# Performance work log

Hardware: AMD Instinct MI355X
Metric: run time of the kernel (lower is better)

The kernel has to match this reference:

```python
import jax, jax.numpy as jnp
import numpy as np

BS, L, ED = 4, 2048, 1024
D = ED // 2          # time_embedding_dim = 512
ANG_HID = D // 4     # AngleEmb hidden = 128
T_MAX = 1010


def _gelu(x):
    return jax.nn.gelu(x, approximate=False)  # torch F.gelu default = exact erf


def _time_embed(t, w1, b1, w2, b2):
    # sinusoidal (diffusion-style, base 10000) + 2-layer MLP; t: [N] float
    half = D // 2
    freqs = jnp.exp(-jnp.log(10000.0) * jnp.arange(half, dtype=jnp.float32) / half)
    a = t[:, None] * freqs[None, :]
    e = jnp.concatenate([jnp.sin(a), jnp.cos(a)], axis=-1)  # [N, D]
    return _gelu(e @ w1 + b1) @ w2 + b2


def _cal_dist(p, aa_seq):
    # p: [bs, L, 3]; ragged per-segment mean pairwise distance.
    # Segments run (cls_idx+1 .. eos_idx-1]; token 0 = cls, token 2 = eos.
    cls = (aa_seq == 0)
    eos = (aa_seq == 2)
    seg = jnp.cumsum(cls.astype(jnp.int32), axis=1)                       # segment id
    valid = (seg > jnp.cumsum(eos.astype(jnp.int32), axis=1)) & ~cls & ~eos
    same = (seg[:, :, None] == seg[:, None, :]) & valid[:, :, None] & valid[:, None, :]
    diff = p[:, :, None, :] - p[:, None, :, :]                            # [bs,L,L,3]
    sq = jnp.sum(diff * diff, axis=-1)
    d = jnp.where(sq > 0, jnp.sqrt(jnp.where(sq > 0, sq, 1.0)), 0.0)      # safe norm
    cnt = jnp.sum(same, axis=-1)                                           # segment size (incl self)
    dist = jnp.where(valid, jnp.sum(d * same, axis=-1) / jnp.maximum(cnt, 1), 0.0)
    return dist[..., None]                                                 # [bs,L,1]


def setup_inputs() -> dict:
    key = jax.random.key(0)
    ks = jax.random.split(key, 26)
    # build ragged aa_seq: repeated [cls=0, residues in [3,25), eos=2], pad token 1
    rng = np.random.default_rng(0)
    aa = np.ones((BS, L), dtype=np.int64)
    pad = np.ones((BS, L), dtype=bool)
    for b in range(BS):
        i = 0
        while i < L - 8:
            seg = int(rng.integers(16, 64))
            seg = min(seg, L - i - 2)
            aa[b, i] = 0
            aa[b, i + 1:i + 1 + seg] = rng.integers(3, 25, size=seg)
            aa[b, i + 1 + seg] = 2
            pad[b, i:i + 2 + seg] = False
            i += seg + 2
    s = 0.05
    inp = {
        "pos": jax.random.normal(ks[0], (BS, L, 3, 3), jnp.float32) * 5.0,
        "angle": jax.random.uniform(ks[1], (BS, L, 6), jnp.float32, -3.14, 3.14),
        "padding_mask": jnp.asarray(pad),
        "mask_aa": jax.random.bernoulli(ks[2], 0.15, (BS, L, 1)),
        "mask_pos": jax.random.bernoulli(ks[3], 0.15, (BS, L, 1)),
        "mask_angle": jax.random.bernoulli(ks[4], 0.15, (BS, L, 1)),
        "angle_mask": jax.random.bernoulli(ks[5], 0.9, (BS, L, 3)),
        "bond_angle_mask": jax.random.bernoulli(ks[6], 0.9, (BS, L, 3)),
        "time_pos": jax.random.randint(ks[7], (BS, L), 0, T_MAX).astype(jnp.float32),
        "time_angle": jnp.zeros((BS, L, 6), jnp.float32),  # overwritten in fwd (dim-2 path)
        "aa_seq": jnp.asarray(aa),
        # parameters ([in, out] layout; torch Linear bias=False unless noted)
        "ang_w1": jax.random.normal(ks[8], (1, ANG_HID), jnp.float32) * 0.5,
        "ang_w2": jax.random.normal(ks[9], (ANG_HID, D), jnp.float32) * s,
        "pos_w1": jax.random.normal(ks[10], (1, 1), jnp.float32) * 0.5,
        "pos_w2": jax.random.normal(ks[11], (1, D), jnp.float32) * s,
        "te_w1": jax.random.normal(ks[12], (D, D), jnp.float32) * s,
        "te_b1": jnp.zeros((D,), jnp.float32),
        "te_w2": jax.random.normal(ks[13], (D, D), jnp.float32) * s,
        "te_b2": jnp.zeros((D,), jnp.float32),
        "angproj_w": jax.random.normal(ks[14], (6 * D, D), jnp.float32) * s,
        "angproj_b": jnp.zeros((D,), jnp.float32),
        "posproj_w": jax.random.normal(ks[15], (D, D), jnp.float32) * s,
        "posproj_b": jnp.zeros((D,), jnp.float32),
        "cls_w": jax.random.normal(ks[16], (1, ED), jnp.float32) * s,
        "eos_w": jax.random.normal(ks[17], (1, ED), jnp.float32) * s,
        "unkang_w": jax.random.normal(ks[18], (1, D), jnp.float32) * s,
        "unkpos_w": jax.random.normal(ks[19], (1, D), jnp.float32) * s,
    }
    return inp


def reference(pos, angle, padding_mask, mask_aa, mask_pos, mask_angle,
              angle_mask, bond_angle_mask, time_pos, time_angle, aa_seq,
              ang_w1, ang_w2, pos_w1, pos_w2,
              te_w1, te_b1, te_w2, te_b2,
              angproj_w, angproj_b, posproj_w, posproj_b,
              cls_w, eos_w, unkang_w, unkpos_w):
    bs, nnode, _ = angle.shape
    amask = jnp.concatenate([angle_mask[:, :, :3], bond_angle_mask], axis=-1)  # [bs,L,6]
    ang = jnp.where(amask, angle, 0.0).reshape(bs, -1, 1)                      # [bs,6L,1]
    cls_mask = (aa_seq == 0)[..., None]
    eos_mask = (aa_seq == 2)[..., None]

    angle_feat = _gelu(ang @ ang_w1) @ ang_w2                                  # [bs,6L,D]
    angle_feat = jnp.where(amask.reshape(bs, -1, 1), angle_feat, unkang_w[0])

    dist = _cal_dist(pos[:, :, 1, :], aa_seq)                                  # [bs,L,1]
    pos_feat = _gelu(dist @ pos_w1) @ pos_w2                                   # [bs,L,D]
    pos_mask = ~(cls_mask | eos_mask)
    pos_feat = jnp.where(pos_mask, pos_feat, unkpos_w[0])

    # time_pos is 2-D -> [bs,L,1]; time_angle := time_pos repeated to [bs,L,6]
    ta = jnp.where(amask, jnp.broadcast_to(time_pos[..., None], (bs, nnode, 6)), 0.0)
    temb_pos = _time_embed(time_pos.reshape(-1), te_w1, te_b1, te_w2, te_b2).reshape(bs, -1, D)
    temb_ang = _time_embed(ta.reshape(-1), te_w1, te_b1, te_w2, te_b2).reshape(bs, -1, D)
    t0_emb = _time_embed(jnp.zeros((1,), jnp.float32), te_w1, te_b1, te_w2, te_b2)[0]  # all-zero t rows are identical

    t_mask = mask_angle & ~cls_mask & ~eos_mask                                # [bs,L,1]
    temb_ang = jnp.where(jnp.tile(t_mask, (1, 6, 1)), temb_ang, t0_emb)        # torch .repeat(1,6,1)
    temb_pos = jnp.where(t_mask, temb_pos, t0_emb)
    angle_feat = angle_feat + temb_ang
    pos_feat = pos_feat + temb_pos

    angle_feat = angle_feat.reshape(bs, nnode, 6 * D) @ angproj_w + angproj_b  # [bs,L,D]
    pos_feat = pos_feat @ posproj_w + posproj_b                                # [bs,L,D]
    node = jnp.concatenate([angle_feat, pos_feat], axis=-1)                    # [bs,L,ED]
    node = jnp.where(cls_mask, cls_w[0], node)
    node = jnp.where(eos_mask, eos_w[0], node)
    node = jnp.where(padding_mask[..., None], 0.0, node)
    return node
```

## Files before the change

### kernel.cpp

```cpp
#include <hip/hip_runtime.h>
#include <hip/hip_bf16.h>
#include <cstdint>
#include <cstddef>

#define BSZ 4
#define SEQL 2048
#define DDIM 512
#define AHID 128
#define NROWS (BSZ*SEQL)
#define NANG (NROWS*6)
#define KCAT 768
#define NTT 1024

typedef __attribute__((ext_vector_type(8))) short short8;
typedef __attribute__((ext_vector_type(4))) float f32x4;
typedef __hip_bfloat16 bf16;

__device__ __forceinline__ float gelu_f(float x){
  return 0.5f * x * (1.0f + erff(x * 0.7071067811865475f));
}

__device__ __forceinline__ void gload16(const void* g, void* l){
  __builtin_amdgcn_global_load_lds(
      (const __attribute__((address_space(1))) unsigned int*)g,
      (__attribute__((address_space(3))) unsigned int*)l,
      16, 0, 0);
}

__device__ __forceinline__ unsigned int packbf2(float a, float b){
  __hip_bfloat16 ha = __float2bfloat16(a), hb = __float2bfloat16(b);
  return (unsigned int)(*(unsigned short*)&ha) | ((unsigned int)(*(unsigned short*)&hb) << 16);
}

__global__ void pre_kernel(const int* __restrict__ aa, const float* __restrict__ pos,
                           float4* __restrict__ pk,
                           const float* __restrict__ te_b2,
                           const float* __restrict__ angproj_w, const float* __restrict__ posproj_w,
                           const float* __restrict__ unkang, const float* __restrict__ pos_w2,
                           float* __restrict__ U, float* __restrict__ Wg,
                           float* __restrict__ qb){
  int blk = blockIdx.x, tid = threadIdx.x;
  if (blk == 0){
    int b = tid >> 6, lane = tid & 63;
    const int CH = SEQL/64;
    int base = b*SEQL + lane*CH;
    int av[CH];
    int lc=0, le=0;
    #pragma unroll
    for (int i=0;i<CH;i++){ int a=aa[base+i]; av[i]=a; lc += (a==0); le += (a==2); }
    int pc=lc, pe=le;
    #pragma unroll
    for (int off=1; off<64; off<<=1){
      int tc = __shfl_up(pc, off);
      int te = __shfl_up(pe, off);
      if (lane >= off){ pc += tc; pe += te; }
    }
    int c = pc - lc, eo = pe - le;
    #pragma unroll
    for (int i=0;i<CH;i++){
      int a = av[i];
      c += (a==0); eo += (a==2);
      bool valid = (c>eo) && (a!=0) && (a!=2);
      float4 q;
      q.x = pos[(size_t)(base+i)*9+3];
      q.y = pos[(size_t)(base+i)*9+4];
      q.z = pos[(size_t)(base+i)*9+5];
      q.w = valid ? (float)c : -1.f;
      pk[base+i] = q;
    }
    return;
  }
  int q = blk - 1;
  if (q < 96){
    int j = q >> 4, rem = q & 15;
    int nc = rem >> 3, dc = rem & 7;
    int n = nc*256 + tid, d0 = dc*64;
    float s = 0.f;
    #pragma unroll 4
    for (int i=0;i<64;i++)
      s += unkang[d0+i] * angproj_w[((size_t)(j*512 + d0+i))*512 + n];
    atomicAdd(U + j*512 + n, s);
    return;
  }
  q -= 96;
  if (q < 16){
    int nc = q >> 3, dc = q & 7;
    int n = nc*256 + tid, d0 = dc*64;
    float s = 0.f;
    #pragma unroll 4
    for (int i=0;i<64;i++)
      s += pos_w2[d0+i] * posproj_w[(size_t)(d0+i)*512 + n];
    atomicAdd(Wg + n, s);
    return;
  }
  q -= 16;
  {
    int j = q >> 4, rem = q & 15;
    int nc = rem >> 3, dc = rem & 7;
    int n = nc*256 + tid, d0 = dc*64;
    const float* W = (j<6) ? (angproj_w + (size_t)(j*512)*512) : posproj_w;
    float s = 0.f;
    #pragma unroll 4
    for (int i=0;i<64;i++)
      s += te_b2[d0+i] * W[(size_t)(d0+i)*512 + n];
    atomicAdd(qb + j*512 + n, s);
  }
}

#define NB_ANGH 3072
#define NB_SIN  256
#define NB_TR   2208
#define NB_PREP 32
#define NB_DIST 2048
#define NB_TOTAL (NB_ANGH+NB_SIN+NB_TR+NB_PREP+NB_DIST)

__device__ void do_transpose(const float* __restrict__ W, bf16* __restrict__ Wt,
                             int K, int q, float (*tsh)[33]){
  int k0 = (q >> 4)*32, n0 = (q & 15)*32;
  int tx = threadIdx.x & 31, ty = threadIdx.x >> 5;
  #pragma unroll
  for (int i=0;i<32;i+=8)
    tsh[ty+i][tx] = W[(size_t)(k0+ty+i)*512 + n0+tx];
  __syncthreads();
  #pragma unroll
  for (int i=0;i<32;i+=8)
    Wt[(size_t)(n0+ty+i)*K + k0+tx] = __float2bfloat16(tsh[tx][ty+i]);
}

__global__ void prologue_kernel(const float* __restrict__ angle,
                                const int* __restrict__ angm, const int* __restrict__ bondm,
                                const int* __restrict__ mask_angle, const int* __restrict__ aa,
                                const int* __restrict__ padm,
                                const float* __restrict__ ang_w1,
                                const float* __restrict__ te_w1, const float* __restrict__ te_w2,
                                const float* __restrict__ ang_w2, const float* __restrict__ angproj_w,
                                const float* __restrict__ posproj_w,
                                const float4* __restrict__ pk,
                                bf16* __restrict__ Hang, bf16* __restrict__ et,
                                bf16* __restrict__ tw1t, bf16* __restrict__ apjt,
                                bf16* __restrict__ ppjt, bf16* __restrict__ w2b,
                                bf16* __restrict__ tw2b,
                                unsigned char* __restrict__ amb, unsigned char* __restrict__ scb,
                                float* __restrict__ dist){
  __shared__ float tsh[32][33];
  int blk = blockIdx.x;
  int tid = threadIdx.x;
  if (blk < NB_ANGH){
    int gidx = blk*256 + tid;
    int row = gidx >> 4;
    int kb = (gidx & 15) * 8;
    int bq = row / (SEQL*6);
    int rr = row - bq*(SEQL*6);
    int l = rr / 6, j = rr - l*6;
    int bl = bq*SEQL + l;
    int m = (j<3) ? angm[bl*3+j] : bondm[bl*3+(j-3)];
    float x = m ? angle[bl*6+j] : 0.f;
    float4 w0 = *(const float4*)(ang_w1+kb);
    float4 w1v = *(const float4*)(ang_w1+kb+4);
    uint4 st;
    st.x = packbf2(gelu_f(x*w0.x),  gelu_f(x*w0.y));
    st.y = packbf2(gelu_f(x*w0.z),  gelu_f(x*w0.w));
    st.z = packbf2(gelu_f(x*w1v.x), gelu_f(x*w1v.y));
    st.w = packbf2(gelu_f(x*w1v.z), gelu_f(x*w1v.w));
    *(uint4*)(Hang + (size_t)row*AHID + kb) = st;
    return;
  }
  blk -= NB_ANGH;
  if (blk < NB_SIN){
    int gidx = blk*256 + tid;
    int row = gidx >> 6;
    int db = (gidx & 63) * 8;
    float t = (float)row;
    float v[8];
    #pragma unroll
    for (int i=0;i<8;i++){
      int d = db + i;
      int k = d & 255;
      float f = exp2f(-0.05190512648262f * (float)k);
      float a = t * f;
      v[i] = (d < 256) ? __sinf(a) : __cosf(a);
    }
    uint4 st;
    st.x = packbf2(v[0],v[1]); st.y = packbf2(v[2],v[3]);
    st.z = packbf2(v[4],v[5]); st.w = packbf2(v[6],v[7]);
    *(uint4*)(et + (size_t)row*DDIM + db) = st;
    return;
  }
  blk -= NB_SIN;
  if (blk < NB_TR){
    if (blk < 256)       do_transpose(te_w1, tw1t, 512, blk, tsh);
    else if (blk < 1792) do_transpose(angproj_w, apjt, 3072, blk-256, tsh);
    else if (blk < 2048) do_transpose(posproj_w, ppjt, 512, blk-1792, tsh);
    else if (blk < 2080){
      int gidx = (blk-2048)*256 + tid;
      float4 a0 = *(const float4*)(ang_w2 + (size_t)gidx*8);
      float4 a1 = *(const float4*)(ang_w2 + (size_t)gidx*8 + 4);
      uint4 st;
      st.x = packbf2(a0.x,a0.y); st.y = packbf2(a0.z,a0.w);
      st.z = packbf2(a1.x,a1.y); st.w = packbf2(a1.z,a1.w);
      *(uint4*)(w2b + (size_t)gidx*8) = st;
    } else {
      int gidx = (blk-2080)*256 + tid;
      float4 a0 = *(const float4*)(te_w2 + (size_t)gidx*8);
      float4 a1 = *(const float4*)(te_w2 + (size_t)gidx*8 + 4);
      uint4 st;
      st.x = packbf2(a0.x,a0.y); st.y = packbf2(a0.z,a0.w);
      st.z = packbf2(a1.x,a1.y); st.w = packbf2(a1.z,a1.w);
      *(uint4*)(tw2b + (size_t)gidx*8) = st;
    }
    return;
  }
  blk -= NB_TR;
  if (blk < NB_PREP){
    int bl = blk*256 + tid;
    int b = bl >> 11, l = bl & (SEQL-1);
    int a = aa[bl];
    bool rowOK = (a!=0) && (a!=2) && (padm[bl]==0);
    int ab=0, sb=0;
    #pragma unroll
    for (int j=0;j<6;j++){
      int am = (j<3) ? angm[bl*3+j] : bondm[bl*3+(j-3)];
      int rr = l*6 + j;
      int bl2 = b*SEQL + (rr & (SEQL-1));
      int a2 = aa[bl2];
      bool tm = mask_angle[bl2] && (a2!=0) && (a2!=2);
      bool qs = tm && (am!=0) && rowOK;
      if (am)  ab |= (1<<j);
      if (qs)  sb |= (1<<j);
    }
    if ((mask_angle[bl]!=0) && rowOK) sb |= 64;
    amb[bl] = (unsigned char)ab;
    scb[bl] = (unsigned char)sb;
    return;
  }
  blk -= NB_PREP;
  {
    int gw = blk*4 + (tid >> 6);
    int lane = tid & 63;
    float4 c = pk[gw];
    float out = 0.f;
    if (c.w >= 0.f){
      int rowbase = (gw >> 11) << 11;
      int jlo = gw - 64; if (jlo < rowbase) jlo = rowbase;
      int jhi = gw + 64; if (jhi >= rowbase + SEQL) jhi = rowbase + SEQL - 1;
      float s = 0.f, cnt = 0.f;
      for (int j = gw - 64 + lane; j <= jhi; j += 64){
        if (j < jlo) continue;
        float4 q = pk[j];
        if (q.w == c.w){
          float dx = c.x-q.x, dy = c.y-q.y, dz = c.z-q.z;
          float sq = dx*dx+dy*dy+dz*dz;
          s += (sq>0.f) ? sqrtf(sq) : 0.f;
          cnt += 1.f;
        }
      }
      #pragma unroll
      for (int off=32; off>0; off>>=1){
        s   += __shfl_down(s, off);
        cnt += __shfl_down(cnt, off);
      }
      out = s / fmaxf(cnt, 1.f);
    }
    if (lane==0) dist[gw] = out;
  }
}

struct EpiArgs {
  const float* bias;
  const unsigned char* amb;
  const unsigned char* scb;
  const float* U;
  const float* Y;
  const float* tp;
  const int* aa;
  const int* pad;
  const float* cls;
  const float* eos;
  float* outF;
  bf16* outB;
  int cnt;
  int coloff;
  int ldc;
};

#define STG_BYTES 12288
#define SMEM_BYTES 49152

template<int EPI>
__device__ __forceinline__ void gemm_core(const char* gA, const char* gB,
                                          int K, int bm, int bn, const EpiArgs& ea, char* smem){
  const int tid = threadIdx.x;
  const int w = tid >> 6, lane = tid & 63;
  const bool doB = (w < 4);
  const int wm = (w>>1)*32, wn = (w&1)*32;
  const int lm = lane & 15, kq = lane >> 4;
  const int sw = kq ^ ((lm>>1)&3);
  const int NT = K >> 5;

  f32x4 acc[2][2];
  #pragma unroll
  for (int i=0;i<2;i++)
    #pragma unroll
    for (int j=0;j<2;j++) acc[i][j] = (f32x4){0.f,0.f,0.f,0.f};

  #pragma unroll
  for (int s=0; s<3; ++s){
    char* base = smem + s*STG_BYTES;
    gload16(gA + (size_t)s*64, base + w*1024);
    if (doB) gload16(gB + (size_t)s*64, base + 8192 + w*1024);
  }

  for (int t = 0; t < NT; ++t){
    char* cur = smem + (t&3)*STG_BYTES;
    if (t+3 < NT){
      char* nxt = smem + ((t+3)&3)*STG_BYTES;
      gload16(gA + (size_t)(t+3)*64, nxt + w*1024);
      if (doB) gload16(gB + (size_t)(t+3)*64, nxt + 8192 + w*1024);
    }
    int ia = NT-1-t; if (ia > 3) ia = 3;
    if (doB){
      if      (ia==3) __asm__ volatile("s_waitcnt vmcnt(6)" ::: "memory");
      else if (ia==2) __asm__ volatile("s_waitcnt vmcnt(4)" ::: "memory");
      else if (ia==1) __asm__ volatile("s_waitcnt vmcnt(2)" ::: "memory");
      else            __asm__ volatile("s_waitcnt vmcnt(0)" ::: "memory");
    } else {
      if      (ia==3) __asm__ volatile("s_waitcnt vmcnt(3)" ::: "memory");
      else if (ia==2) __asm__ volatile("s_waitcnt vmcnt(2)" ::: "memory");
      else if (ia==1) __asm__ volatile("s_waitcnt vmcnt(1)" ::: "memory");
      else            __asm__ volatile("s_waitcnt vmcnt(0)" ::: "memory");
    }
    __builtin_amdgcn_s_barrier();
    short8 af[2], bfr[2];
    #pragma unroll
    for (int tt=0;tt<2;tt++) af[tt]  = *(const short8*)(cur + (wm+tt*16+lm)*64 + sw*16);
    #pragma unroll
    for (int tt=0;tt<2;tt++) bfr[tt] = *(const short8*)(cur + 8192 + (wn+tt*16+lm)*64 + sw*16);
    #pragma unroll
    for (int mt=0;mt<2;mt++)
      #pragma unroll
      for (int nt=0;nt<2;nt++)
        acc[mt][nt] = __builtin_amdgcn_mfma_f32_16x16x32_bf16(af[mt], bfr[nt], acc[mt][nt], 0, 0, 0);
    __builtin_amdgcn_s_barrier();
  }

  float* eps = (float*)smem + w*576;
  const int erow = lane >> 2;
  const int ecg  = (lane & 3) * 8;
  #pragma unroll
  for (int mt=0; mt<2; mt++){
    #pragma unroll
    for (int nt=0; nt<2; nt++)
      #pragma unroll
      for (int rr=0; rr<4; rr++)
        eps[(kq*4+rr)*36 + nt*16 + lm] = acc[mt][nt][rr];
    __asm__ volatile("s_waitcnt lgkmcnt(0)" ::: "memory");
    float4 t0v = *(float4*)(eps + erow*36 + ecg);
    float4 t1v = *(float4*)(eps + erow*36 + ecg + 4);
    float v[8] = {t0v.x,t0v.y,t0v.z,t0v.w,t1v.x,t1v.y,t1v.z,t1v.w};
    __asm__ volatile("s_waitcnt lgkmcnt(0)" ::: "memory");
    int row = bm + wm + mt*16 + erow;
    int col = bn + wn + ecg;

    if (EPI==0 || EPI==1){
      float4 b0 = *(const float4*)(ea.bias+col), b1 = *(const float4*)(ea.bias+col+4);
      float bb[8] = {b0.x,b0.y,b0.z,b0.w,b1.x,b1.y,b1.z,b1.w};
      #pragma unroll
      for (int i=0;i<8;i++){
        v[i] += bb[i];
        if (EPI==0) v[i] = gelu_f(v[i]);
      }
      uint4 st;
      st.x = packbf2(v[0],v[1]); st.y = packbf2(v[2],v[3]);
      st.z = packbf2(v[4],v[5]); st.w = packbf2(v[6],v[7]);
      *(uint4*)(ea.outB + (size_t)row*ea.ldc + col) = st;
    } else if (EPI==4){
      uint4 st;
      st.x = packbf2(v[0],v[1]); st.y = packbf2(v[2],v[3]);
      st.z = packbf2(v[4],v[5]); st.w = packbf2(v[6],v[7]);
      *(uint4*)(ea.outB + (size_t)row*ea.ldc + col + ea.coloff) = st;
    } else if (EPI==5){
      float4 b0 = *(const float4*)(ea.bias+col), b1 = *(const float4*)(ea.bias+col+4);
      v[0]+=b0.x; v[1]+=b0.y; v[2]+=b0.z; v[3]+=b0.w;
      v[4]+=b1.x; v[5]+=b1.y; v[6]+=b1.z; v[7]+=b1.w;
      int ab = ea.amb[row], sc = ea.scb[row];
      int trow = (int)ea.tp[row];
      #pragma unroll
      for (int j=0;j<6;j++){
        float mU = ((ab>>j)&1) ? 0.f : 1.f;
        const float* Up = ea.U + j*512 + col;
        float4 u0=*(const float4*)Up, u1=*(const float4*)(Up+4);
        int idx = ((sc>>j)&1) ? trow : 0;
        const float* yp = ea.Y + ((size_t)j*NTT + idx)*512 + col;
        float4 y0=*(const float4*)yp, y1=*(const float4*)(yp+4);
        v[0]+=mU*u0.x+y0.x; v[1]+=mU*u0.y+y0.y;
        v[2]+=mU*u0.z+y0.z; v[3]+=mU*u0.w+y0.w;
        v[4]+=mU*u1.x+y1.x; v[5]+=mU*u1.y+y1.y;
        v[6]+=mU*u1.z+y1.z; v[7]+=mU*u1.w+y1.w;
      }
      int a = ea.aa[row];
      if (a==0){
        float4 c0 = *(const float4*)(ea.cls+col), c1 = *(const float4*)(ea.cls+col+4);
        v[0]=c0.x;v[1]=c0.y;v[2]=c0.z;v[3]=c0.w;v[4]=c1.x;v[5]=c1.y;v[6]=c1.z;v[7]=c1.w;
      } else if (a==2){
        float4 c0 = *(const float4*)(ea.eos+col), c1 = *(const float4*)(ea.eos+col+4);
        v[0]=c0.x;v[1]=c0.y;v[2]=c0.z;v[3]=c0.w;v[4]=c1.x;v[5]=c1.y;v[6]=c1.z;v[7]=c1.w;
      }
      if (ea.pad[row]){
        #pragma unroll
        for (int i=0;i<8;i++) v[i]=0.f;
      }
      *(float4*)(ea.outF + (size_t)row*ea.ldc + col)     = make_float4(v[0],v[1],v[2],v[3]);
      *(float4*)(ea.outF + (size_t)row*ea.ldc + col + 4) = make_float4(v[4],v[5],v[6],v[7]);
    } else {
      if (row < ea.cnt){
        float4 b0 = *(const float4*)(ea.bias+col), b1 = *(const float4*)(ea.bias+col+4);
        v[0]+=b0.x; v[1]+=b0.y; v[2]+=b0.z; v[3]+=b0.w;
        v[4]+=b1.x; v[5]+=b1.y; v[6]+=b1.z; v[7]+=b1.w;
        float* dst = ea.outF + (size_t)row*ea.ldc + col;
        *(float4*)dst     = make_float4(v[0],v[1],v[2],v[3]);
        *(float4*)(dst+4) = make_float4(v[4],v[5],v[6],v[7]);
      }
    }
  }
}

__device__ __forceinline__ void mk_addrs(const bf16* A, size_t lda, int bm,
                                         const bf16* Bt, size_t ldb, int bn,
                                         const char*& gA, const char*& gB){
  int tid = threadIdx.x;
  int w = tid >> 6, lane = tid & 63;
  int r = w*16 + (lane>>2);
  int cg = (lane&3) ^ ((r>>1)&3);
  gA = (const char*)(A + (size_t)(bm+r)*lda + cg*8);
  gB = (const char*)(Bt + (size_t)(bn+r)*ldb + cg*8);
}

__launch_bounds__(512, 8)
__global__ void te1_wcat_q_kernel(const bf16* __restrict__ et, const bf16* __restrict__ tw1t,
                                  EpiArgs eaH,
                                  const bf16* __restrict__ apjt, const bf16* __restrict__ ppjt,
                                  const bf16* __restrict__ w2b, const bf16* __restrict__ tw2b,
                                  EpiArgs eaW, bf16* __restrict__ QT){
  __shared__ __align__(16) char smem[SMEM_BYTES];
  int id = blockIdx.x;
  const char *gA, *gB;
  if (id < 64){
    int m = id >> 3, n = id & 7;
    mk_addrs(et, 512, m*128, tw1t, 512, n*64, gA, gB);
    gemm_core<0>(gA, gB, 512, m*128, n*64, eaH, smem);
  } else if (id < 112){
    int q = id - 64;
    int j = q >> 3, m = (q >> 1) & 3, n = q & 1;
    mk_addrs(apjt, 3072, m*128, w2b, 512, n*64, gA, gB);
    gA += (size_t)j*512*2;
    eaW.coloff = j*128;
    gemm_core<4>(gA, gB, 512, m*128, n*64, eaW, smem);
  } else {
    int q = id - 112;
    int j = q >> 5, rem = q & 31;
    int m = rem >> 3, n = rem & 7;
    if (j < 6){
      mk_addrs(apjt, 3072, m*128, tw2b, 512, n*64, gA, gB);
      gA += (size_t)j*512*2;
    } else {
      mk_addrs(ppjt, 512, m*128, tw2b, 512, n*64, gA, gB);
    }
    EpiArgs ea{};
    ea.outB = QT + (size_t)j*DDIM*DDIM; ea.ldc = DDIM; ea.coloff = 0;
    gemm_core<4>(gA, gB, 512, m*128, n*64, ea, smem);
  }
}

__launch_bounds__(512, 8)
__global__ void yt_kernel(const bf16* __restrict__ H1, const bf16* __restrict__ QT,
                          const float* __restrict__ qb, float* __restrict__ YT){
  __shared__ __align__(16) char smem[SMEM_BYTES];
  int id = blockIdx.x;
  int jj = id >> 6, rem = id & 63;
  int mt = rem >> 3, nt = rem & 7;
  const char *gA, *gB;
  mk_addrs(H1, 512, mt*128, QT + (size_t)jj*DDIM*DDIM, 512, nt*64, gA, gB);
  EpiArgs ea{};
  ea.bias = qb + jj*512;
  ea.cnt = NTT;
  ea.outF = YT + (size_t)jj*NTT*512;
  ea.ldc = 512;
  gemm_core<7>(gA, gB, 512, mt*128, nt*64, ea, smem);
}

__launch_bounds__(512, 8)
__global__ void proj_kernel(const bf16* __restrict__ Hang, const bf16* __restrict__ Wcat,
                            EpiArgs eaA,
                            const int* __restrict__ aa, const int* __restrict__ padm,
                            const unsigned char* __restrict__ scb,
                            const float* __restrict__ YT,
                            const float* __restrict__ dist, const float* __restrict__ time_pos,
                            const float* __restrict__ pw1, const float* __restrict__ Wg,
                            const float* __restrict__ bp,
                            const float* __restrict__ cls, const float* __restrict__ eos,
                            float* __restrict__ out){
  __shared__ __align__(16) char smem[SMEM_BYTES];
  int id = blockIdx.x;
  if (id < 512){
    int c = id & 7, q = id >> 3;
    int n = q & 7, mh = q >> 3;
    int m = mh*8 + c;
    const char *gA, *gB;
    mk_addrs(Hang, KCAT, m*128, Wcat, KCAT, n*64, gA, gB);
    gemm_core<5>(gA, gB, KCAT, m*128, n*64, eaA, smem);
    return;
  }
  int gidx = (id-512)*512 + threadIdx.x;
  int row = gidx >> 6;
  int db = (gidx & 63) * 8;
  int a = aa[row];
  float v[8];
  if (a==0 || a==2){
    const float* src = ((a==0) ? cls : eos) + DDIM + db;
    float4 c0 = *(const float4*)src, c1 = *(const float4*)(src+4);
    v[0]=c0.x;v[1]=c0.y;v[2]=c0.z;v[3]=c0.w;v[4]=c1.x;v[5]=c1.y;v[6]=c1.z;v[7]=c1.w;
  } else {
    int sc = scb[row];
    float g = gelu_f(dist[row]*pw1[0]);
    int idx = (sc & 64) ? (int)time_pos[row] : 0;
    const float* yp = YT + ((size_t)6*NTT + idx)*512 + db;
    float4 g0 = *(const float4*)(Wg+db),  g1 = *(const float4*)(Wg+db+4);
    float4 y0 = *(const float4*)yp,       y1 = *(const float4*)(yp+4);
    float4 b0 = *(const float4*)(bp+db),  b1 = *(const float4*)(bp+db+4);
    v[0]=g*g0.x+y0.x+b0.x; v[1]=g*g0.y+y0.y+b0.y;
    v[2]=g*g0.z+y0.z+b0.z; v[3]=g*g0.w+y0.w+b0.w;
    v[4]=g*g1.x+y1.x+b1.x; v[5]=g*g1.y+y1.y+b1.y;
    v[6]=g*g1.z+y1.z+b1.z; v[7]=g*g1.w+y1.w+b1.w;
  }
  if (padm[row]){
    #pragma unroll
    for (int i=0;i<8;i++) v[i]=0.f;
  }
  float* dst = out + (size_t)row*1024 + DDIM + db;
  *(float4*)dst     = make_float4(v[0],v[1],v[2],v[3]);
  *(float4*)(dst+4) = make_float4(v[4],v[5],v[6],v[7]);
}

extern "C" void kernel_launch(void* const* d_in, const int* in_sizes, int n_in,
                              void* d_out, int out_size, void* d_ws, size_t ws_size,
                              hipStream_t stream){
  const float* pos        = (const float*)d_in[0];
  const float* angle      = (const float*)d_in[1];
  const int*   padm       = (const int*)d_in[2];
  const int*   mask_angle = (const int*)d_in[5];
  const int*   angle_mask = (const int*)d_in[6];
  const int*   bond_mask  = (const int*)d_in[7];
  const float* time_pos   = (const float*)d_in[8];
  const int*   aa         = (const int*)d_in[10];
  const float* ang_w1     = (const float*)d_in[11];
  const float* ang_w2     = (const float*)d_in[12];
  const float* pos_w1     = (const float*)d_in[13];
  const float* pos_w2     = (const float*)d_in[14];
  const float* te_w1      = (const float*)d_in[15];
  const float* te_b1      = (const float*)d_in[16];
  const float* te_w2      = (const float*)d_in[17];
  const float* te_b2      = (const float*)d_in[18];
  const float* angproj_w  = (const float*)d_in[19];
  const float* angproj_b  = (const float*)d_in[20];
  const float* posproj_w  = (const float*)d_in[21];
  const float* posproj_b  = (const float*)d_in[22];
  const float* cls_w      = (const float*)d_in[23];
  const float* eos_w      = (const float*)d_in[24];
  const float* unkang     = (const float*)d_in[25];

  char* ws = (char*)d_ws;
  size_t off = 0;
  auto alloc = [&](size_t bytes)->char*{
    char* p = ws + off;
    off += (bytes + 255) & ~(size_t)255;
    return p;
  };
  float* U      = (float*)alloc((size_t)6*DDIM*4);
  float* Wg     = (float*)alloc((size_t)DDIM*4);
  float* qb     = (float*)alloc((size_t)7*DDIM*4);
  size_t zbytes = (size_t)((char*)qb - (char*)U) + 7*DDIM*4;
  float* dist   = (float*)alloc((size_t)NROWS*4);
  float4* pk    = (float4*)alloc((size_t)NROWS*16);
  unsigned char* amb  = (unsigned char*)alloc(NROWS);
  unsigned char* scb  = (unsigned char*)alloc(NROWS);
  bf16*  et     = (bf16*) alloc((size_t)NTT*DDIM*2);
  bf16*  H1     = (bf16*) alloc((size_t)NTT*DDIM*2);
  bf16*  Hang   = (bf16*) alloc((size_t)NANG*AHID*2);
  bf16*  tw1t   = (bf16*) alloc((size_t)DDIM*DDIM*2);
  bf16*  apjt   = (bf16*) alloc((size_t)DDIM*6*DDIM*2);
  bf16*  ppjt   = (bf16*) alloc((size_t)DDIM*DDIM*2);
  bf16*  w2b    = (bf16*) alloc((size_t)AHID*DDIM*2);
  bf16*  tw2b   = (bf16*) alloc((size_t)DDIM*DDIM*2);
  bf16*  Wcat   = (bf16*) alloc((size_t)DDIM*KCAT*2);
  bf16*  QT     = (bf16*) alloc((size_t)7*DDIM*DDIM*2);
  float* YT     = (float*)alloc((size_t)7*NTT*512*4);

  float* out = (float*)d_out;
  dim3 b256(256), b512(512);

  hipMemsetAsync(U, 0, zbytes, stream);

  pre_kernel<<<dim3(225), b256, 0, stream>>>(aa, pos, pk,
      te_b2, angproj_w, posproj_w, unkang, pos_w2, U, Wg, qb);

  prologue_kernel<<<dim3(NB_TOTAL), b256, 0, stream>>>(
      angle, angle_mask, bond_mask, mask_angle, aa, padm, ang_w1,
      te_w1, te_w2, ang_w2, angproj_w, posproj_w, pk,
      Hang, et, tw1t, apjt, ppjt, w2b, tw2b, amb, scb, dist);

  EpiArgs eaH{}; eaH.bias = te_b1; eaH.outB = H1; eaH.ldc = DDIM;
  EpiArgs eaW{}; eaW.outB = Wcat; eaW.ldc = KCAT;
  te1_wcat_q_kernel<<<dim3(336), b512, 0, stream>>>(et, tw1t, eaH,
      apjt, ppjt, w2b, tw2b, eaW, QT);

  yt_kernel<<<dim3(448), b512, 0, stream>>>(H1, QT, qb, YT);

  EpiArgs eaA{};
  eaA.bias = angproj_b; eaA.amb = amb; eaA.scb = scb; eaA.U = U;
  eaA.Y = YT; eaA.tp = time_pos;
  eaA.aa = aa; eaA.pad = padm; eaA.cls = cls_w; eaA.eos = eos_w;
  eaA.outF = out; eaA.ldc = 1024;
  proj_kernel<<<dim3(1536), b512, 0, stream>>>(Hang, Wcat, eaA,
      aa, padm, scb, YT, dist, time_pos, pos_w1, Wg, posproj_b, cls_w, eos_w, out);
}
```

Before: 197.1 us.

## Fold pre_kernel into prologue and move distance computation into GEMM kernel

Removes the separate pre_kernel launch by running the segment scan (now one block per batch with a cross-wave prefix) and the weight-vector matvecs as extra block ranges inside the prologue kernel. The per-row distance computation moves from the prologue into the te1/Wcat/QT GEMM kernel as 1024 extra blocks of 8 waves, since it depends on the scan output and must run in a later launch. This cuts one kernel launch and the serial dependency it creates. The GEMM kernel now has a larger, mixed grid, and its heavy blocks share the device with lightweight distance blocks.

```diff
diff --git a/kernel.cpp b/kernel.cpp
--- a/kernel.cpp
+++ b/kernel.cpp
@@ -32,87 +32,13 @@
   return (unsigned int)(*(unsigned short*)&ha) | ((unsigned int)(*(unsigned short*)&hb) << 16);
 }
 
-__global__ void pre_kernel(const int* __restrict__ aa, const float* __restrict__ pos,
-                           float4* __restrict__ pk,
-                           const float* __restrict__ te_b2,
-                           const float* __restrict__ angproj_w, const float* __restrict__ posproj_w,
-                           const float* __restrict__ unkang, const float* __restrict__ pos_w2,
-                           float* __restrict__ U, float* __restrict__ Wg,
-                           float* __restrict__ qb){
-  int blk = blockIdx.x, tid = threadIdx.x;
-  if (blk == 0){
-    int b = tid >> 6, lane = tid & 63;
-    const int CH = SEQL/64;
-    int base = b*SEQL + lane*CH;
-    int av[CH];
-    int lc=0, le=0;
-    #pragma unroll
-    for (int i=0;i<CH;i++){ int a=aa[base+i]; av[i]=a; lc += (a==0); le += (a==2); }
-    int pc=lc, pe=le;
-    #pragma unroll
-    for (int off=1; off<64; off<<=1){
-      int tc = __shfl_up(pc, off);
-      int te = __shfl_up(pe, off);
-      if (lane >= off){ pc += tc; pe += te; }
-    }
-    int c = pc - lc, eo = pe - le;
-    #pragma unroll
-    for (int i=0;i<CH;i++){
-      int a = av[i];
-      c += (a==0); eo += (a==2);
-      bool valid = (c>eo) && (a!=0) && (a!=2);
-      float4 q;
-      q.x = pos[(size_t)(base+i)*9+3];
-      q.y = pos[(size_t)(base+i)*9+4];
-      q.z = pos[(size_t)(base+i)*9+5];
-      q.w = valid ? (float)c : -1.f;
-      pk[base+i] = q;
-    }
-    return;
-  }
-  int q = blk - 1;
-  if (q < 96){
-    int j = q >> 4, rem = q & 15;
-    int nc = rem >> 3, dc = rem & 7;
-    int n = nc*256 + tid, d0 = dc*64;
-    float s = 0.f;
-    #pragma unroll 4
-    for (int i=0;i<64;i++)
-      s += unkang[d0+i] * angproj_w[((size_t)(j*512 + d0+i))*512 + n];
-    atomicAdd(U + j*512 + n, s);
-    return;
-  }
-  q -= 96;
-  if (q < 16){
-    int nc = q >> 3, dc = q & 7;
-    int n = nc*256 + tid, d0 = dc*64;
-    float s = 0.f;
-    #pragma unroll 4
-    for (int i=0;i<64;i++)
-      s += pos_w2[d0+i] * posproj_w[(size_t)(d0+i)*512 + n];
-    atomicAdd(Wg + n, s);
-    return;
-  }
-  q -= 16;
-  {
-    int j = q >> 4, rem = q & 15;
-    int nc = rem >> 3, dc = rem & 7;
-    int n = nc*256 + tid, d0 = dc*64;
-    const float* W = (j<6) ? (angproj_w + (size_t)(j*512)*512) : posproj_w;
-    float s = 0.f;
-    #pragma unroll 4
-    for (int i=0;i<64;i++)
-      s += te_b2[d0+i] * W[(size_t)(d0+i)*512 + n];
-    atomicAdd(qb + j*512 + n, s);
-  }
-}
-
+#define NB_SCAN 4
 #define NB_ANGH 3072
 #define NB_SIN  256
 #define NB_TR   2208
 #define NB_PREP 32
-#define NB_DIST 2048
-#define NB_TOTAL (NB_ANGH+NB_SIN+NB_TR+NB_PREP+NB_DIST)
+#define NB_MV   224
+#define NB_TOTAL (NB_SCAN+NB_ANGH+NB_SIN+NB_TR+NB_PREP+NB_MV)
 
 __device__ void do_transpose(const float* __restrict__ W, bf16* __restrict__ Wt,
                              int K, int q, float (*tsh)[33]){
@@ -131,20 +57,59 @@
                                 const int* __restrict__ angm, const int* __restrict__ bondm,
                                 const int* __restrict__ mask_angle, const int* __restrict__ aa,
                                 const int* __restrict__ padm,
+                                const float* __restrict__ pos,
                                 const float* __restrict__ ang_w1,
                                 const float* __restrict__ te_w1, const float* __restrict__ te_w2,
+                                const float* __restrict__ te_b2,
                                 const float* __restrict__ ang_w2, const float* __restrict__ angproj_w,
                                 const float* __restrict__ posproj_w,
-                                const float4* __restrict__ pk,
+                                const float* __restrict__ unkang, const float* __restrict__ pos_w2,
+                                float4* __restrict__ pk,
                                 bf16* __restrict__ Hang, bf16* __restrict__ et,
                                 bf16* __restrict__ tw1t, bf16* __restrict__ apjt,
                                 bf16* __restrict__ ppjt, bf16* __restrict__ w2b,
                                 bf16* __restrict__ tw2b,
                                 unsigned char* __restrict__ amb, unsigned char* __restrict__ scb,
-                                float* __restrict__ dist){
+                                float* __restrict__ U, float* __restrict__ Wg,
+                                float* __restrict__ qb){
   __shared__ float tsh[32][33];
+  __shared__ int wcs[4], wes[4];
   int blk = blockIdx.x;
   int tid = threadIdx.x;
+  if (blk < NB_SCAN){
+    int b = blk;
+    int base = b*SEQL + tid*8;
+    int av[8];
+    int lc=0, le=0;
+    #pragma unroll
+    for (int i=0;i<8;i++){ int a=aa[base+i]; av[i]=a; lc += (a==0); le += (a==2); }
+    int lane = tid & 63, wid = tid >> 6;
+    int pc=lc, pe=le;
+    #pragma unroll
+    for (int off=1; off<64; off<<=1){
+      int tc = __shfl_up(pc, off);
+      int te = __shfl_up(pe, off);
+      if (lane >= off){ pc += tc; pe += te; }
+    }
+    if (lane == 63){ wcs[wid] = pc; wes[wid] = pe; }
+    __syncthreads();
+    int c = pc - lc, eo = pe - le;
+    for (int w2=0; w2<wid; w2++){ c += wcs[w2]; eo += wes[w2]; }
+    #pragma unroll
+    for (int i=0;i<8;i++){
+      int a = av[i];
+      c += (a==0); eo += (a==2);
+      bool valid = (c>eo) && (a!=0) && (a!=2);
+      float4 q;
+      q.x = pos[(size_t)(base+i)*9+3];
+      q.y = pos[(size_t)(base+i)*9+4];
+      q.z = pos[(size_t)(base+i)*9+5];
+      q.w = valid ? (float)c : -1.f;
+      pk[base+i] = q;
+    }
+    return;
+  }
+  blk -= NB_SCAN;
   if (blk < NB_ANGH){
     int gidx = blk*256 + tid;
     int row = gidx >> 4;
@@ -235,33 +200,41 @@
   }
   blk -= NB_PREP;
   {
-    int gw = blk*4 + (tid >> 6);
-    int lane = tid & 63;
-    float4 c = pk[gw];
-    float out = 0.f;
-    if (c.w >= 0.f){
-      int rowbase = (gw >> 11) << 11;
-      int jlo = gw - 64; if (jlo < rowbase) jlo = rowbase;
-      int jhi = gw + 64; if (jhi >= rowbase + SEQL) jhi = rowbase + SEQL - 1;
-      float s = 0.f, cnt = 0.f;
-      for (int j = gw - 64 + lane; j <= jhi; j += 64){
-        if (j < jlo) continue;
-        float4 q = pk[j];
-        if (q.w == c.w){
-          float dx = c.x-q.x, dy = c.y-q.y, dz = c.z-q.z;
-          float sq = dx*dx+dy*dy+dz*dz;
-          s += (sq>0.f) ? sqrtf(sq) : 0.f;
-          cnt += 1.f;
-        }
-      }
-      #pragma unroll
-      for (int off=32; off>0; off>>=1){
-        s   += __shfl_down(s, off);
-        cnt += __shfl_down(cnt, off);
-      }
-      out = s / fmaxf(cnt, 1.f);
-    }
-    if (lane==0) dist[gw] = out;
+    int q = blk;
+    if (q < 96){
+      int j = q >> 4, rem = q & 15;
+      int nc = rem >> 3, dc = rem & 7;
+      int n = nc*256 + tid, d0 = dc*64;
+      float s = 0.f;
+      #pragma unroll 4
+      for (int i=0;i<64;i++)
+        s += unkang[d0+i] * angproj_w[((size_t)(j*512 + d0+i))*512 + n];
+      atomicAdd(U + j*512 + n, s);
+      return;
+    }
+    q -= 96;
+    if (q < 16){
+      int nc = q >> 3, dc = q & 7;
+      int n = nc*256 + tid, d0 = dc*64;
+      float s = 0.f;
+      #pragma unroll 4
+      for (int i=0;i<64;i++)
+        s += pos_w2[d0+i] * posproj_w[(size_t)(d0+i)*512 + n];
+      atomicAdd(Wg + n, s);
+      return;
+    }
+    q -= 16;
+    {
+      int j = q >> 4, rem = q & 15;
+      int nc = rem >> 3, dc = rem & 7;
+      int n = nc*256 + tid, d0 = dc*64;
+      const float* W = (j<6) ? (angproj_w + (size_t)(j*512)*512) : posproj_w;
+      float s = 0.f;
+      #pragma unroll 4
+      for (int i=0;i<64;i++)
+        s += te_b2[d0+i] * W[(size_t)(d0+i)*512 + n];
+      atomicAdd(qb + j*512 + n, s);
+    }
   }
 }
 
@@ -440,7 +413,8 @@
                                   EpiArgs eaH,
                                   const bf16* __restrict__ apjt, const bf16* __restrict__ ppjt,
                                   const bf16* __restrict__ w2b, const bf16* __restrict__ tw2b,
-                                  EpiArgs eaW, bf16* __restrict__ QT){
+                                  EpiArgs eaW, bf16* __restrict__ QT,
+                                  const float4* __restrict__ pk, float* __restrict__ dist){
   __shared__ __align__(16) char smem[SMEM_BYTES];
   int id = blockIdx.x;
   const char *gA, *gB;
@@ -448,14 +422,18 @@
     int m = id >> 3, n = id & 7;
     mk_addrs(et, 512, m*128, tw1t, 512, n*64, gA, gB);
     gemm_core<0>(gA, gB, 512, m*128, n*64, eaH, smem);
-  } else if (id < 112){
+    return;
+  }
+  if (id < 112){
     int q = id - 64;
     int j = q >> 3, m = (q >> 1) & 3, n = q & 1;
     mk_addrs(apjt, 3072, m*128, w2b, 512, n*64, gA, gB);
     gA += (size_t)j*512*2;
     eaW.coloff = j*128;
     gemm_core<4>(gA, gB, 512, m*128, n*64, eaW, smem);
-  } else {
+    return;
+  }
+  if (id < 336){
     int q = id - 112;
     int j = q >> 5, rem = q & 31;
     int m = rem >> 3, n = rem & 7;
@@ -468,6 +446,37 @@
     EpiArgs ea{};
     ea.outB = QT + (size_t)j*DDIM*DDIM; ea.ldc = DDIM; ea.coloff = 0;
     gemm_core<4>(gA, gB, 512, m*128, n*64, ea, smem);
+    return;
+  }
+  {
+    int tid = threadIdx.x;
+    int gw = (id-336)*8 + (tid >> 6);
+    int lane = tid & 63;
+    float4 c = pk[gw];
+    float out = 0.f;
+    if (c.w >= 0.f){
+      int rowbase = (gw >> 11) << 11;
+      int jlo = gw - 64; if (jlo < rowbase) jlo = rowbase;
+      int jhi = gw + 64; if (jhi >= rowbase + SEQL) jhi = rowbase + SEQL - 1;
+      float s = 0.f, cnt = 0.f;
+      for (int j = gw - 64 + lane; j <= jhi; j += 64){
+        if (j < jlo) continue;
+        float4 q = pk[j];
+        if (q.w == c.w){
+          float dx = c.x-q.x, dy = c.y-q.y, dz = c.z-q.z;
+          float sq = dx*dx+dy*dy+dz*dz;
+          s += (sq>0.f) ? sqrtf(sq) : 0.f;
+          cnt += 1.f;
+        }
+      }
+      #pragma unroll
+      for (int off=32; off>0; off>>=1){
+        s   += __shfl_down(s, off);
+        cnt += __shfl_down(cnt, off);
+      }
+      out = s / fmaxf(cnt, 1.f);
+    }
+    if (lane==0) dist[gw] = out;
   }
 }
 
@@ -600,18 +609,15 @@
 
   hipMemsetAsync(U, 0, zbytes, stream);
 
-  pre_kernel<<<dim3(225), b256, 0, stream>>>(aa, pos, pk,
-      te_b2, angproj_w, posproj_w, unkang, pos_w2, U, Wg, qb);
-
   prologue_kernel<<<dim3(NB_TOTAL), b256, 0, stream>>>(
-      angle, angle_mask, bond_mask, mask_angle, aa, padm, ang_w1,
-      te_w1, te_w2, ang_w2, angproj_w, posproj_w, pk,
-      Hang, et, tw1t, apjt, ppjt, w2b, tw2b, amb, scb, dist);
+      angle, angle_mask, bond_mask, mask_angle, aa, padm, pos, ang_w1,
+      te_w1, te_w2, te_b2, ang_w2, angproj_w, posproj_w, unkang, pos_w2,
+      pk, Hang, et, tw1t, apjt, ppjt, w2b, tw2b, amb, scb, U, Wg, qb);
 
   EpiArgs eaH{}; eaH.bias = te_b1; eaH.outB = H1; eaH.ldc = DDIM;
   EpiArgs eaW{}; eaW.outB = Wcat; eaW.ldc = KCAT;
-  te1_wcat_q_kernel<<<dim3(336), b512, 0, stream>>>(et, tw1t, eaH,
-      apjt, ppjt, w2b, tw2b, eaW, QT);
+  te1_wcat_q_kernel<<<dim3(1360), b512, 0, stream>>>(et, tw1t, eaH,
+      apjt, ppjt, w2b, tw2b, eaW, QT, pk, dist);
 
   yt_kernel<<<dim3(448), b512, 0, stream>>>(H1, QT, qb, YT);
 
```

After: 179.2 us (median of 2 runs). -9.1%, faster.
